# Optimization experiments

Hardware: AMD Instinct MI355X
Metric: run time of the kernel (lower is better)

## Reference

```python
import jax, jax.numpy as jnp
import numpy as np


def setup_inputs() -> dict:
    key = jax.random.key(0)
    k1, k2 = jax.random.split(key)
    B, C, L, K = 16, 64, 4096, 1024
    x = jax.random.normal(k1, (B, C, L), dtype=jnp.float32)
    codebook = jax.random.normal(k2, (K, C), dtype=jnp.float32)
    return {"x": x, "codebook": codebook}


def reference(x, codebook):
    # x: (B, C, L), codebook: (K, C)
    B, C, L = x.shape
    xt = jnp.transpose(x, (0, 2, 1))  # (B, L, C)

    # Squared Euclidean distances (argmin is invariant to the sqrt in torch.cdist)
    x2 = jnp.sum(xt * xt, axis=-1, keepdims=True)            # (B, L, 1)
    w2 = jnp.sum(codebook * codebook, axis=-1)               # (K,)
    xw = jnp.einsum("blc,kc->blk", xt, codebook)             # (B, L, K)
    d2 = x2 - 2.0 * xw + w2                                   # (B, L, K)
    min_encoding_indices = jnp.argmin(d2, axis=-1)            # (B, L)

    quant = codebook[min_encoding_indices]                    # (B, L, C)

    commitment_loss = jnp.mean((jax.lax.stop_gradient(quant) - xt) ** 2)
    codebook_loss = jnp.mean((quant - jax.lax.stop_gradient(xt)) ** 2)

    # Straight-through estimator
    quant_out = xt + jax.lax.stop_gradient(quant - xt)        # (B, L, C)
    quant_out = jnp.transpose(quant_out, (0, 2, 1))           # (B, C, L)

    return quant_out, codebook_loss, commitment_loss, min_encoding_indices
```

## Files before the change

### kernel.cpp

```cpp
#include <hip/hip_runtime.h>

#define BATCH 16
#define CH    64
#define LEN   4096
#define NCODE 1024
#define NPTS  (BATCH * LEN)
#define NPART 512
#define UNITB 24576

typedef float float2v __attribute__((ext_vector_type(2)));
typedef float float4v __attribute__((ext_vector_type(4)));
typedef short short8  __attribute__((ext_vector_type(8)));
typedef float f32x16  __attribute__((ext_vector_type(16)));
typedef unsigned int uint32;

__device__ __forceinline__ unsigned short f2bf(float f) {
    uint32 u = __builtin_bit_cast(uint32, f);
    u += 0x7fffu + ((u >> 16) & 1u);
    return (unsigned short)(u >> 16);
}
__device__ __forceinline__ float bf2f(unsigned short h) {
    uint32 u = ((uint32)h) << 16;
    return __builtin_bit_cast(float, u);
}

__global__ __launch_bounds__(256) void vq_prep(const float* __restrict__ cb,
                                               short* __restrict__ cbf2,
                                               float* __restrict__ w2tab) {
    __shared__ float tile[64][65];
    __shared__ float s2p[4][64];
    const int k0 = blockIdx.x * 64;
    const int t  = threadIdx.x;
#pragma unroll
    for (int it = 0; it < 4; ++it) {
        int idx = it * 256 + t, row = idx >> 4, q = idx & 15;
        *(float4v*)&tile[row][q * 4] =
            *(const float4v*)&cb[(size_t)(k0 + row) * CH + q * 4];
    }
    __syncthreads();

    const int j  = t & 63;
    const int cq = t >> 6;
    const int k  = k0 + j, T = k >> 5, row = k & 31;
    const int Tp = (T < 16) ? (T * 2) : ((T - 16) * 2 + 1);
    float s2 = 0.f;
#pragma unroll
    for (int cc = 0; cc < 16; ++cc) {
        float xv = tile[j][cq * 16 + cc];
        s2 = fmaf(xv, xv, s2);
        unsigned short h1 = f2bf(xv); float f1 = bf2f(h1);
        float r1 = xv - f1;
        unsigned short h2 = f2bf(r1); float f2 = bf2f(h2);
        float r2 = r1 - f2;
        unsigned short h3 = f2bf(r2);
        int g = cc >> 3, i = cc & 7;
        int lane = g * 32 + row;
        size_t base = ((size_t)Tp * 12 + cq * 3) * 512 + lane * 8 + i;
        cbf2[base]        = (short)h1;
        cbf2[base + 512]  = (short)h2;
        cbf2[base + 1024] = (short)h3;
    }
    s2p[cq][j] = s2;
    __syncthreads();
    if (t < 64) {
        float s2t = ((s2p[0][t] + s2p[1][t]) + (s2p[2][t] + s2p[3][t]));
        int kk = k0 + t, TT = kk >> 5, rr = kk & 31;
        int hi = (rr >> 2) & 1, r = (rr & 3) + 4 * (rr >> 3);
        w2tab[((size_t)TT * 2 + hi) * 16 + r] = s2t;
    }
}

__device__ __forceinline__ void epi(const f32x16& acc, int Tg, int g,
                                    float& bestc, int& bestk,
                                    const float* w2s) {
    const float4v* wt = (const float4v*)(w2s + ((size_t)Tg * 2 + g) * 16);
    float4v w0 = wt[0], w1 = wt[1], w2v = wt[2], w3 = wt[3];
    float wr[16] = {w0.x, w0.y, w0.z, w0.w, w1.x, w1.y, w1.z, w1.w,
                    w2v.x, w2v.y, w2v.z, w2v.w, w3.x, w3.y, w3.z, w3.w};
    int kbase = Tg * 32 + 4 * g;
#pragma unroll
    for (int r = 0; r < 16; ++r) {
        float cost = fmaf(-2.0f, acc[r], wr[r]);
        int kg = kbase + (r & 3) + 8 * (r >> 2);
        if (cost < bestc) { bestc = cost; bestk = kg; }
    }
}

__global__ void __launch_bounds__(512)
__attribute__((amdgpu_waves_per_eu(4, 4)))
vq_argmin(const float*  __restrict__ x,
          const float*  __restrict__ cb,
          const short*  __restrict__ cbf2,
          const float*  __restrict__ w2tab,
          float*        __restrict__ quant,
          float*        __restrict__ idx_out,
          double*       __restrict__ partial) {
    __shared__ __attribute__((aligned(16))) char  ring[2 * UNITB];
    __shared__ __attribute__((aligned(16))) float w2s[NCODE];
    __shared__ float  smc[8][32];
    __shared__ int    smk[8][32];
    __shared__ int    fidx[128];
    __shared__ double sds[128];

    const int t   = threadIdx.x;
    const int l   = t & 63;
    const int w   = __builtin_amdgcn_readfirstlane(t >> 6);
    const int h2  = w >> 2;
    const int ptl = (w & 3) * 32 + (l & 31);
    const int g   = l >> 5;
    const int p0  = blockIdx.x * 128;
    const int b   = p0 >> 12;
    const int l0  = p0 & (LEN - 1);

    float* xs = (float*)ring;

#pragma unroll
    for (int it = 0; it < 4; ++it) {
        int fi = it * 512 + t, c = fi >> 5, p4 = fi & 31;
        *(float4v*)&xs[c * 128 + 4 * p4] =
            *(const float4v*)&x[((size_t)b * CH + c) * LEN + l0 + 4 * p4];
    }
    w2s[t]       = w2tab[t];
    w2s[t + 512] = w2tab[t + 512];
    __syncthreads();

    short8 B1[4], B2[4], B3[4];
    float x2p = 0.f;
#pragma unroll
    for (int s = 0; s < 4; ++s) {
#pragma unroll
        for (int i = 0; i < 8; ++i) {
            int c = s * 16 + g * 8 + i;
            float xv = xs[c * 128 + ptl];
            x2p = fmaf(xv, xv, x2p);
            unsigned short h1v = f2bf(xv); float f1 = bf2f(h1v);
            float r1 = xv - f1;
            unsigned short h2v = f2bf(r1); float f2 = bf2f(h2v);
            float r2 = r1 - f2;
            unsigned short h3v = f2bf(r2);
            B1[s][i] = (short)h1v; B2[s][i] = (short)h2v; B3[s][i] = (short)h3v;
        }
    }
    const float x2 = x2p + __shfl_xor(x2p, 32, 64);
    __syncthreads();

    const float4v* gsrc = (const float4v*)cbf2;

    float4v sA0, sA1, sA2, sB0, sB1, sB2;
    sA0 = gsrc[t]; sA1 = gsrc[512 + t]; sA2 = gsrc[1024 + t];
    {
        float4v* d = (float4v*)ring;
        d[t] = sA0; d[512 + t] = sA1; d[1024 + t] = sA2;
    }
    sA0 = gsrc[1536 + t]; sA1 = gsrc[2048 + t]; sA2 = gsrc[2560 + t];
    asm volatile("s_waitcnt lgkmcnt(0)" ::: "memory");
    __builtin_amdgcn_s_barrier();
    asm volatile("" ::: "memory");

    float bestc = 3.4e38f;
    int   bestk = 0;

    auto STEP = [&](int tt, float4v& cu0, float4v& cu1, float4v& cu2,
                    float4v& nx0, float4v& nx1, float4v& nx2) {
        if (tt + 2 < 16) {
            const float4v* gs = gsrc + (size_t)(tt + 2) * 1536;
            nx0 = gs[t]; nx1 = gs[512 + t]; nx2 = gs[1024 + t];
        }
        const short* bp = (const short*)&ring[(tt & 1) * UNITB] + h2 * 6144;
        f32x16 acc1 = {0.f,0.f,0.f,0.f,0.f,0.f,0.f,0.f,
                       0.f,0.f,0.f,0.f,0.f,0.f,0.f,0.f};
        f32x16 acc2 = acc1;
#pragma unroll
        for (int s = 0; s < 4; ++s) {
            const short* fb = bp + (s * 3) * 512 + l * 8;
            short8 A1 = *(const short8*)(fb);
            short8 A2 = *(const short8*)(fb + 512);
            short8 A3 = *(const short8*)(fb + 1024);
            acc1 = __builtin_amdgcn_mfma_f32_32x32x16_bf16(A1, B1[s], acc1, 0, 0, 0);
            acc2 = __builtin_amdgcn_mfma_f32_32x32x16_bf16(A1, B2[s], acc2, 0, 0, 0);
            acc1 = __builtin_amdgcn_mfma_f32_32x32x16_bf16(A2, B1[s], acc1, 0, 0, 0);
            acc2 = __builtin_amdgcn_mfma_f32_32x32x16_bf16(A1, B3[s], acc2, 0, 0, 0);
            acc1 = __builtin_amdgcn_mfma_f32_32x32x16_bf16(A3, B1[s], acc1, 0, 0, 0);
            acc2 = __builtin_amdgcn_mfma_f32_32x32x16_bf16(A2, B2[s], acc2, 0, 0, 0);
        }
        f32x16 acc = acc1 + acc2;
        epi(acc, h2 * 16 + tt, g, bestc, bestk, w2s);
        if (tt + 1 < 16) {
            float4v* d = (float4v*)&ring[((tt + 1) & 1) * UNITB];
            d[t] = cu0; d[512 + t] = cu1; d[1024 + t] = cu2;
        }
        asm volatile("s_waitcnt lgkmcnt(0)" ::: "memory");
        __builtin_amdgcn_s_barrier();
        asm volatile("" ::: "memory");
    };

    for (int tp = 0; tp < 8; ++tp) {
        STEP(2 * tp,     sA0, sA1, sA2, sB0, sB1, sB2);
        STEP(2 * tp + 1, sB0, sB1, sB2, sA0, sA1, sA2);
    }

    {
        float ob = __shfl_xor(bestc, 32, 64);
        int   ok = __shfl_xor(bestk, 32, 64);
        if (ob < bestc || (ob == bestc && ok < bestk)) { bestc = ob; bestk = ok; }
    }
    if (l < 32) { smc[w][l] = bestc; smk[w][l] = bestk; }
    __syncthreads();
    if (w < 4 && l < 32) {
        float ob = smc[w + 4][l];
        int   ok = smk[w + 4][l];
        if (ob < bestc || (ob == bestc && ok < bestk)) { bestc = ob; bestk = ok; }
        idx_out[p0 + w * 32 + l] = (float)bestk;
        fidx[w * 32 + l] = bestk;
        sds[w * 32 + l] = (double)x2 + (double)bestc;
    }
    __syncthreads();

    {
        const int pt = t & 127;
        const int cq = t >> 7;
        const int k  = fidx[pt];
        const float4v* src = (const float4v*)(cb + (size_t)k * CH + cq * 16);
        float4v v0 = src[0], v1 = src[1], v2 = src[2], v3 = src[3];
        float vr[16] = {v0.x, v0.y, v0.z, v0.w, v1.x, v1.y, v1.z, v1.w,
                        v2.x, v2.y, v2.z, v2.w, v3.x, v3.y, v3.z, v3.w};
#pragma unroll
        for (int j = 0; j < 16; ++j) {
            int c = cq * 16 + j;
            quant[((size_t)b * CH + c) * LEN + l0 + pt] = vr[j];
        }
    }

    if (t == 0) {
        double s = 0.0;
        for (int i = 0; i < 128; ++i) s += sds[i];
        partial[blockIdx.x] = s;
    }
}

__global__ __launch_bounds__(256) void vq_loss(const double* __restrict__ partial,
                                               float*        __restrict__ losses) {
    __shared__ double sred[256];
    double v = 0.0;
#pragma unroll
    for (int i = 0; i < NPART / 256; ++i) v += partial[threadIdx.x + 256 * i];
    sred[threadIdx.x] = v;
    __syncthreads();
    for (int s = 128; s > 0; s >>= 1) {
        if (threadIdx.x < s) sred[threadIdx.x] += sred[threadIdx.x + s];
        __syncthreads();
    }
    if (threadIdx.x == 0) {
        float loss = (float)(sred[0] / (double)((size_t)NPTS * CH));
        losses[0] = loss;
        losses[1] = loss;
    }
}

extern "C" void kernel_launch(void* const* d_in, const int* in_sizes, int n_in,
                              void* d_out, int out_size, void* d_ws, size_t ws_size,
                              hipStream_t stream) {
    const float* x  = (const float*)d_in[0];
    const float* cb = (const float*)d_in[1];
    float* out = (float*)d_out;

    float* quant_out = out;
    float* losses    = out + (size_t)BATCH * CH * LEN;
    float* idx_out   = losses + 2;

    double* partial = (double*)d_ws;
    float*  w2tab   = (float*)((char*)d_ws + 4096);
    short*  cbf2    = (short*)((char*)d_ws + 16384);

    vq_prep<<<16, 256, 0, stream>>>(cb, cbf2, w2tab);
    vq_argmin<<<NPTS / 128, 512, 0, stream>>>(x, cb, cbf2, w2tab,
                                              quant_out, idx_out, partial);
    vq_loss<<<1, 256, 0, stream>>>(partial, losses);
}
```

Before: 70.87 us.

## Triple-buffer LDS ring, single MFMA accumulator, setprio, alias reduction scratch

Grows the shared-memory ring from two to three codebook tiles, indexed modulo 3, and places the reduction scratch arrays inside the ring behind an extra barrier to save LDS. It replaces the two interleaved MFMA accumulators with one dependent chain, raises wave priority around the MFMA loop, and changes the launch bounds from waves_per_eu(4,4) to a min-blocks hint of 2. The aim is fewer registers and better overlap of loads with matrix math. The costs are a serialized MFMA dependency chain, more LDS per block, and a changed occupancy target.

```diff
diff --git a/kernel.cpp b/kernel.cpp
--- a/kernel.cpp
+++ b/kernel.cpp
@@ -86,8 +86,7 @@
     }
 }
 
-__global__ void __launch_bounds__(512)
-__attribute__((amdgpu_waves_per_eu(4, 4)))
+__global__ void __launch_bounds__(512, 2)
 vq_argmin(const float*  __restrict__ x,
           const float*  __restrict__ cb,
           const short*  __restrict__ cbf2,
@@ -95,12 +94,13 @@
           float*        __restrict__ quant,
           float*        __restrict__ idx_out,
           double*       __restrict__ partial) {
-    __shared__ __attribute__((aligned(16))) char  ring[2 * UNITB];
+    __shared__ __attribute__((aligned(16))) char  ring[3 * UNITB];
     __shared__ __attribute__((aligned(16))) float w2s[NCODE];
-    __shared__ float  smc[8][32];
-    __shared__ int    smk[8][32];
-    __shared__ int    fidx[128];
-    __shared__ double sds[128];
+
+    float*  smc  = (float*)ring;
+    int*    smk  = (int*)(ring + 1024);
+    int*    fidx = (int*)(ring + 2048);
+    double* sds  = (double*)(ring + 2560);
 
     const int t   = threadIdx.x;
     const int l   = t & 63;
@@ -166,27 +166,27 @@
             const float4v* gs = gsrc + (size_t)(tt + 2) * 1536;
             nx0 = gs[t]; nx1 = gs[512 + t]; nx2 = gs[1024 + t];
         }
-        const short* bp = (const short*)&ring[(tt & 1) * UNITB] + h2 * 6144;
-        f32x16 acc1 = {0.f,0.f,0.f,0.f,0.f,0.f,0.f,0.f,
-                       0.f,0.f,0.f,0.f,0.f,0.f,0.f,0.f};
-        f32x16 acc2 = acc1;
+        const short* bp = (const short*)&ring[(tt % 3) * UNITB] + h2 * 6144;
+        f32x16 acc = {0.f,0.f,0.f,0.f,0.f,0.f,0.f,0.f,
+                      0.f,0.f,0.f,0.f,0.f,0.f,0.f,0.f};
+        __builtin_amdgcn_s_setprio(1);
 #pragma unroll
         for (int s = 0; s < 4; ++s) {
             const short* fb = bp + (s * 3) * 512 + l * 8;
             short8 A1 = *(const short8*)(fb);
             short8 A2 = *(const short8*)(fb + 512);
             short8 A3 = *(const short8*)(fb + 1024);
-            acc1 = __builtin_amdgcn_mfma_f32_32x32x16_bf16(A1, B1[s], acc1, 0, 0, 0);
-            acc2 = __builtin_amdgcn_mfma_f32_32x32x16_bf16(A1, B2[s], acc2, 0, 0, 0);
-            acc1 = __builtin_amdgcn_mfma_f32_32x32x16_bf16(A2, B1[s], acc1, 0, 0, 0);
-            acc2 = __builtin_amdgcn_mfma_f32_32x32x16_bf16(A1, B3[s], acc2, 0, 0, 0);
-            acc1 = __builtin_amdgcn_mfma_f32_32x32x16_bf16(A3, B1[s], acc1, 0, 0, 0);
-            acc2 = __builtin_amdgcn_mfma_f32_32x32x16_bf16(A2, B2[s], acc2, 0, 0, 0);
-        }
-        f32x16 acc = acc1 + acc2;
+            acc = __builtin_amdgcn_mfma_f32_32x32x16_bf16(A1, B1[s], acc, 0, 0, 0);
+            acc = __builtin_amdgcn_mfma_f32_32x32x16_bf16(A1, B2[s], acc, 0, 0, 0);
+            acc = __builtin_amdgcn_mfma_f32_32x32x16_bf16(A2, B1[s], acc, 0, 0, 0);
+            acc = __builtin_amdgcn_mfma_f32_32x32x16_bf16(A1, B3[s], acc, 0, 0, 0);
+            acc = __builtin_amdgcn_mfma_f32_32x32x16_bf16(A3, B1[s], acc, 0, 0, 0);
+            acc = __builtin_amdgcn_mfma_f32_32x32x16_bf16(A2, B2[s], acc, 0, 0, 0);
+        }
+        __builtin_amdgcn_s_setprio(0);
         epi(acc, h2 * 16 + tt, g, bestc, bestk, w2s);
         if (tt + 1 < 16) {
-            float4v* d = (float4v*)&ring[((tt + 1) & 1) * UNITB];
+            float4v* d = (float4v*)&ring[((tt + 1) % 3) * UNITB];
             d[t] = cu0; d[512 + t] = cu1; d[1024 + t] = cu2;
         }
         asm volatile("s_waitcnt lgkmcnt(0)" ::: "memory");
@@ -204,11 +204,12 @@
         int   ok = __shfl_xor(bestk, 32, 64);
         if (ob < bestc || (ob == bestc && ok < bestk)) { bestc = ob; bestk = ok; }
     }
-    if (l < 32) { smc[w][l] = bestc; smk[w][l] = bestk; }
+    __syncthreads();
+    if (l < 32) { smc[w * 32 + l] = bestc; smk[w * 32 + l] = bestk; }
     __syncthreads();
     if (w < 4 && l < 32) {
-        float ob = smc[w + 4][l];
-        int   ok = smk[w + 4][l];
+        float ob = smc[(w + 4) * 32 + l];
+        int   ok = smk[(w + 4) * 32 + l];
         if (ob < bestc || (ob == bestc && ok < bestk)) { bestc = ob; bestk = ok; }
         idx_out[p0 + w * 32 + l] = (float)bestk;
         fidx[w * 32 + l] = bestk;
```

After: 62.36 us. 12.0% less time.
